# Kernel tuning notes

Measured on AMD Instinct MI355X. Metric: run time of the kernel, lower is better.

The kernel has to match this reference:

```python
import jax, jax.numpy as jnp
import numpy as np

D = 256; DFF = 1024; H = 8; L = 4; P = 4; NK = 18; NQ = 100; BS = 8; DH = D // H
SHAPES = ((100, 100), (50, 50), (25, 25), (13, 13))   # (H_l, W_l) per level
START = (0, 10000, 12500, 13125); LIN = 13294
PARAM_SHAPES = [
    ("across_in_w", (3 * D, D)), ("across_in_b", (3 * D,)), ("across_out_w", (D, D)), ("across_out_b", (D,)),
    ("within_in_w", (3 * D, D)), ("within_in_b", (3 * D,)), ("within_out_w", (D, D)), ("within_out_b", (D,)),
    ("off_w", (H * L * P * 2, D)), ("off_b", (H * L * P * 2,)), ("aw_w", (H * L * P, D)), ("aw_b", (H * L * P,)),
    ("val_w", (D, D)), ("val_b", (D,)), ("msout_w", (D, D)), ("msout_b", (D,)),
    ("lin1_w", (DFF, D)), ("lin1_b", (DFF,)), ("lin2_w", (D, DFF)), ("lin2_b", (D,)),
    ("lin1p_w", (DFF, D)), ("lin1p_b", (DFF,)), ("lin2p_w", (D, DFF)), ("lin2p_b", (D,)),
]
NORMS = ["across_norm", "within_norm", "norm1", "norm2", "norm2p"]
PNAMES = [n for n, _ in PARAM_SHAPES] + [n + s for n in NORMS for s in ("_g", "_b")]


def setup_inputs():
    ks = iter(jax.random.split(jax.random.key(0), 80))
    rn = lambda s, sc=1.0: jax.random.normal(next(ks), s, jnp.float32) * sc
    inp = {}
    inp["tgt_pose"] = rn((NQ, BS, NK, D))
    inp["tgt_pose_query_pos"] = rn((NQ, BS, NK, D))
    inp["tgt_pose_reference_points"] = jax.random.uniform(next(ks), (NQ * NK, BS, L, 2), jnp.float32)
    inp["memory"] = rn((LIN, BS, D))
    for n, s in PARAM_SHAPES:
        inp[n] = rn(s, 0.02)
    for n in NORMS:
        inp[n + "_g"] = 1.0 + rn((D,), 0.02)
        inp[n + "_b"] = rn((D,), 0.02)
    return inp


def _ln(x, g, b):
    mu = x.mean(-1, keepdims=True)
    xc = x - mu
    return xc * jax.lax.rsqrt((xc * xc).mean(-1, keepdims=True) + 1e-5) * g + b


def _mha(q, k, v, in_w, in_b, out_w, out_b, mask=None):
    # q,k,v: [S,B,D] (torch nn.MultiheadAttention layout)
    S, B, _ = q.shape
    def proj(x, i):
        return (x @ in_w[i * D:(i + 1) * D].T + in_b[i * D:(i + 1) * D]).reshape(-1, B, H, DH).transpose(1, 2, 0, 3)
    qh = proj(q, 0) * (DH ** -0.5); kh = proj(k, 1); vh = proj(v, 2)   # [B,H,S,DH]
    sc = jnp.einsum('bhqd,bhkd->bhqk', qh, kh)
    if mask is not None:
        sc = sc + mask
    o = jnp.einsum('bhqk,bhkd->bhqd', jax.nn.softmax(sc, -1), vh)
    return o.transpose(2, 0, 1, 3).reshape(S, B, D) @ out_w.T + out_b


def _msdeform(query, ref, mem, off_w, off_b, aw_w, aw_b, val_w, val_b, out_w, out_b):
    # query [N,Lq,D], ref [N,Lq,L,2] in [0,1] (x,y), mem [N,LIN,D]
    N, Lq, _ = query.shape
    value = (mem @ val_w.T + val_b).reshape(N, LIN, H, DH).transpose(0, 2, 1, 3)   # [N,H,LIN,DH]
    off = (query @ off_w.T + off_b).reshape(N, Lq, H, L, P, 2)
    aw = jax.nn.softmax((query @ aw_w.T + aw_b).reshape(N, Lq, H, L * P), -1).reshape(N, Lq, H, L, P)
    normalizer = jnp.array([[w, h] for (h, w) in SHAPES], jnp.float32)   # (W_l, H_l)
    loc = ref[:, :, None, :, None, :] + off / normalizer[None, None, None, :, None, :]   # [N,Lq,H,L,P,2]
    lvl_outs = []
    for li, (Hl, Wl) in enumerate(SHAPES):
        v_l = value[:, :, START[li]:START[li] + Hl * Wl]   # [N,H,Hl*Wl,DH]
        g = loc[:, :, :, li]                               # [N,Lq,H,P,2]
        # grid_sample(align_corners=False, padding_mode='zeros') on sampling grid 2*loc-1
        x = g[..., 0] * Wl - 0.5; y = g[..., 1] * Hl - 0.5
        x0 = jnp.floor(x); y0 = jnp.floor(y)
        lx = x - x0; ly = y - y0
        x0i = x0.astype(jnp.int32); y0i = y0.astype(jnp.int32)
        def gather(xi, yi):
            valid = ((xi >= 0) & (xi < Wl) & (yi >= 0) & (yi < Hl)).astype(v_l.dtype)
            idx = jnp.clip(yi, 0, Hl - 1) * Wl + jnp.clip(xi, 0, Wl - 1)   # [N,Lq,H,P]
            it = idx.transpose(0, 2, 1, 3).reshape(N, H, Lq * P)
            vt = jnp.take_along_axis(v_l, it[..., None], axis=2).reshape(N, H, Lq, P, DH)
            return vt * valid.transpose(0, 2, 1, 3)[..., None]
        wx = lx.transpose(0, 2, 1, 3)[..., None]; wy = ly.transpose(0, 2, 1, 3)[..., None]
        samp = (gather(x0i, y0i) * (1 - wx) * (1 - wy) + gather(x0i + 1, y0i) * wx * (1 - wy)
                + gather(x0i, y0i + 1) * (1 - wx) * wy + gather(x0i + 1, y0i + 1) * wx * wy)
        lvl_outs.append(samp)   # [N,H,Lq,P,DH]
    samp = jnp.stack(lvl_outs, 0)   # [L,N,H,Lq,P,DH]
    out = jnp.einsum('lnhqpd,nqhlp->nqhd', samp, aw).reshape(N, Lq, D)
    return out @ out_w.T + out_b


def _forward(tgt, pos, ref, mem, p):
    # 1) across-person self-attention along nq
    qf = tgt.reshape(NQ, BS * NK, D)
    t2 = _mha(qf, qf, qf, p['across_in_w'], p['across_in_b'], p['across_out_w'], p['across_out_b']).reshape(NQ, BS, NK, D)
    tgt = _ln(tgt + t2, p['across_norm_g'], p['across_norm_b'])
    # 2) deformable cross-attention; with_pos_embed mutates tgt in place in the original
    tgt = tgt + pos
    q = tgt.transpose(1, 0, 2, 3).reshape(BS, NQ * NK, D)
    t2 = _msdeform(q, ref.transpose(1, 0, 2, 3), mem.transpose(1, 0, 2),
                   p['off_w'], p['off_b'], p['aw_w'], p['aw_b'], p['val_w'], p['val_b'], p['msout_w'], p['msout_b'])
    t2 = t2.reshape(BS, NQ, NK, D).transpose(1, 0, 2, 3)
    tgt = _ln(tgt + t2, p['norm1_g'], p['norm1_b'])
    # 3) FFN
    t2 = jax.nn.relu(tgt @ p['lin1_w'].T + p['lin1_b']) @ p['lin2_w'].T + p['lin2_b']
    tgt = _ln(tgt + t2, p['norm2_g'], p['norm2_b'])
    # 4) within-pose self-attention (second in-place with_pos_embed)
    tgt = tgt + pos
    qw = tgt.reshape(NQ * BS, NK, D).transpose(1, 0, 2)
    mask = jnp.full((NK, NK), 1e-8, tgt.dtype)   # zero adjacency matrix additive mask
    t2 = _mha(qw, qw, qw, p['within_in_w'], p['within_in_b'], p['within_out_w'], p['within_out_b'], mask)
    t2 = t2.transpose(1, 0, 2).reshape(NQ, BS, NK, D)
    tgt = _ln(tgt + t2, p['within_norm_g'], p['within_norm_b'])
    # 5) late FFN
    t2 = jax.nn.relu(tgt @ p['lin1p_w'].T + p['lin1p_b']) @ p['lin2p_w'].T + p['lin2p_b']
    return _ln(tgt + t2, p['norm2p_g'], p['norm2p_b'])


def reference(tgt_pose, tgt_pose_query_pos, tgt_pose_reference_points, memory, across_in_w, across_in_b, across_out_w, across_out_b, within_in_w, within_in_b, within_out_w, within_out_b, off_w, off_b, aw_w, aw_b, val_w, val_b, msout_w, msout_b, lin1_w, lin1_b, lin2_w, lin2_b, lin1p_w, lin1p_b, lin2p_w, lin2p_b, across_norm_g, across_norm_b, within_norm_g, within_norm_b, norm1_g, norm1_b, norm2_g, norm2_b, norm2p_g, norm2p_b):
    _l = dict(locals())
    p = {n: _l[n] for n in PNAMES}
    return _forward(tgt_pose, tgt_pose_query_pos, tgt_pose_reference_points, memory, p)
```

## Files before the change

kernel.cpp:

```cpp
#include <hip/hip_runtime.h>
#include <cstdint>
#include <cstddef>

constexpr int D_   = 256;
constexpr int NK_  = 18;
constexpr int NQ_  = 100;
constexpr int BS_  = 8;
constexpr int T_   = NQ_ * BS_ * NK_;
constexpr int LIN_ = 13294;
constexpr int LQ_  = NQ_ * NK_;

typedef __attribute__((ext_vector_type(8))) short bfv8;
typedef __attribute__((ext_vector_type(4))) float f32x4;

__device__ __forceinline__ ushort f2b(float f) {
  uint32_t u = __builtin_bit_cast(uint32_t, f);
  u += 0x7fffu + ((u >> 16) & 1u);
  return (ushort)(u >> 16);
}
__device__ __forceinline__ float b2f(ushort h) {
  uint32_t u = ((uint32_t)h) << 16;
  return __builtin_bit_cast(float, u);
}
__device__ __forceinline__ uint pk2(float lo, float hi) {
  return (uint)f2b(lo) | ((uint)f2b(hi) << 16);
}
__device__ __forceinline__ void gload16(const ushort* g, ushort* l) {
  __builtin_amdgcn_global_load_lds(
      (const __attribute__((address_space(1))) void*)g,
      (__attribute__((address_space(3))) void*)l, 16, 0, 0);
}

constexpr int WOF0  = 0;
constexpr int WOF1  = 196608;
constexpr int WOF2  = 393216;
constexpr int WOF3  = 458752;
constexpr int WOF4  = 524288;
constexpr int WOF5  = 589824;
constexpr int WOF6  = 622592;
constexpr int WOF7  = 688128;
constexpr int WOF8  = 753664;
constexpr int WOF9  = 1015808;
constexpr int WOF10 = 1277952;
constexpr int WOF11 = 1540096;
constexpr int WTOT  = 1802240;

__global__ __launch_bounds__(256) void conv_weights(
    const float* __restrict__ w0, const float* __restrict__ w1,
    const float* __restrict__ w2, const float* __restrict__ w3,
    const float* __restrict__ w4, const float* __restrict__ w5,
    const float* __restrict__ w6, const float* __restrict__ w7,
    const float* __restrict__ w8, const float* __restrict__ w9,
    const float* __restrict__ w10, const float* __restrict__ w11,
    ushort* __restrict__ out,
    const float* __restrict__ off_b, const float* __restrict__ aw_b,
    float* __restrict__ oab) {
  if (blockIdx.x == 0) {
    int t = threadIdx.x;
    oab[t] = (t < 256) ? off_b[t] : aw_b[t - 256];
    oab[t + 128] = (t + 128 < 256) ? off_b[t + 128] : aw_b[t - 128];
  }
  int i8 = (blockIdx.x * 256 + threadIdx.x) * 8;
  if (i8 >= WTOT) return;
  const float* src; int off;
  if      (i8 < WOF1)  { src = w0;  off = WOF0; }
  else if (i8 < WOF2)  { src = w1;  off = WOF1; }
  else if (i8 < WOF3)  { src = w2;  off = WOF2; }
  else if (i8 < WOF4)  { src = w3;  off = WOF3; }
  else if (i8 < WOF5)  { src = w4;  off = WOF4; }
  else if (i8 < WOF6)  { src = w5;  off = WOF5; }
  else if (i8 < WOF7)  { src = w6;  off = WOF6; }
  else if (i8 < WOF8)  { src = w7;  off = WOF7; }
  else if (i8 < WOF9)  { src = w8;  off = WOF8; }
  else if (i8 < WOF10) { src = w9;  off = WOF9; }
  else if (i8 < WOF11) { src = w10; off = WOF10; }
  else                 { src = w11; off = WOF11; }
  const float4 v0 = *(const float4*)(src + (i8 - off));
  const float4 v1 = *(const float4*)(src + (i8 - off) + 4);
  uint4 o;
  o.x = pk2(v0.x, v0.y); o.y = pk2(v0.z, v0.w);
  o.z = pk2(v1.x, v1.y); o.w = pk2(v1.z, v1.w);
  *(uint4*)(out + i8) = o;
}

__global__ __launch_bounds__(256) void conv_tgt(
    const float* __restrict__ tgt, ushort* __restrict__ tgtb) {
  int idx = blockIdx.x * 256 + threadIdx.x;
  int r = idx >> 5, c = (idx & 31) * 8;
  if (r >= T_) return;
  const float* p = tgt + (size_t)r * 256 + c;
  float4 v0 = *(const float4*)p, v1 = *(const float4*)(p + 4);
  uint4 o;
  o.x = pk2(v0.x, v0.y); o.y = pk2(v0.z, v0.w);
  o.z = pk2(v1.x, v1.y); o.w = pk2(v1.z, v1.w);
  *(uint4*)(tgtb + (size_t)r * 256 + c) = o;
}

__global__ __launch_bounds__(256) void gemm_vproj(
    const float* __restrict__ Amem, const ushort* __restrict__ W,
    const float* __restrict__ bias, ushort* __restrict__ C, int M) {
  __shared__ ushort As[128 * 32];
  __shared__ ushort Bs[128 * 32];
  const int tid = threadIdx.x;
  const int bm = blockIdx.y * 128, bn = blockIdx.x * 128;
  const int wave = tid >> 6, lane = tid & 63;

  const int srow = wave * 16 + (lane >> 2);
  const float* gAf[2]; ushort* lA[2];
  const ushort* gB[2]; ushort* lB[2];
#pragma unroll
  for (int j = 0; j < 2; ++j) {
    int row = j * 64 + srow;
    int gch = (lane & 3) ^ (row & 3);
    int gm = bm + row; if (gm >= M) gm = M - 1;
    gAf[j] = Amem + (size_t)gm * 256 + gch * 8;
    lA[j] = As + (j * 4 + wave) * 512 + lane * 8;
    gB[j] = W + (size_t)(bn + row) * 256 + gch * 8;
    lB[j] = Bs + (j * 4 + wave) * 512;
  }

  const int wm = (wave >> 1) * 64, wn = (wave & 1) * 64;
  const int fr = lane & 15, fk = lane >> 4;
  const int sw = (fk ^ (fr & 3)) << 3;

  float4 ra[2][2];
#pragma unroll
  for (int j = 0; j < 2; ++j) {
    ra[j][0] = *(const float4*)(gAf[j]);
    ra[j][1] = *(const float4*)(gAf[j] + 4);
  }

  f32x4 acc[4][4] = {};
  for (int k0 = 0; k0 < 256; k0 += 32) {
#pragma unroll
    for (int j = 0; j < 2; ++j) gload16(gB[j] + k0, lB[j]);
#pragma unroll
    for (int j = 0; j < 2; ++j) {
      uint4 o;
      o.x = pk2(ra[j][0].x, ra[j][0].y); o.y = pk2(ra[j][0].z, ra[j][0].w);
      o.z = pk2(ra[j][1].x, ra[j][1].y); o.w = pk2(ra[j][1].z, ra[j][1].w);
      *(uint4*)lA[j] = o;
    }
    __syncthreads();
    if (k0 + 32 < 256) {
#pragma unroll
      for (int j = 0; j < 2; ++j) {
        ra[j][0] = *(const float4*)(gAf[j] + k0 + 32);
        ra[j][1] = *(const float4*)(gAf[j] + k0 + 36);
      }
    }
    bfv8 a[4], b[4];
#pragma unroll
    for (int m = 0; m < 4; ++m)
      a[m] = *(const bfv8*)&As[(wm + m * 16 + fr) * 32 + sw];
#pragma unroll
    for (int n = 0; n < 4; ++n)
      b[n] = *(const bfv8*)&Bs[(wn + n * 16 + fr) * 32 + sw];
#pragma unroll
    for (int m = 0; m < 4; ++m)
#pragma unroll
      for (int n = 0; n < 4; ++n)
        acc[m][n] = __builtin_amdgcn_mfma_f32_16x16x32_bf16(a[m], b[n], acc[m][n], 0, 0, 0);
    __syncthreads();
  }

  const int row0 = (lane >> 4) * 4;
  const int col = lane & 15;
#pragma unroll
  for (int m = 0; m < 4; ++m) {
#pragma unroll
    for (int n = 0; n < 4; ++n) {
      int cn = bn + wn + n * 16 + col;
      float bv = bias[cn];
#pragma unroll
      for (int j = 0; j < 4; ++j) {
        int mg = bm + wm + m * 16 + row0 + j;
        if (mg < M) {
          size_t orow = (size_t)(mg & 7) * LIN_ + (mg >> 3);
          C[orow * 256 + cn] = f2b(acc[m][n][j] + bv);
        }
      }
    }
  }
}

template<int AMODE, int OUTMODE, int BM>
__global__ __launch_bounds__(256) void gemm_mfma(
    const ushort* __restrict__ A, const ushort* __restrict__ W,
    const float* __restrict__ bias, void* __restrict__ Cv,
    int M, int N, int K) {
  constexpr int AJ = BM / 64;
  constexpr int MR = BM / 32;
  __shared__ ushort As[BM * 32];
  __shared__ ushort Bs[128 * 32];
  const int tid = threadIdx.x;
  const int bm = blockIdx.y * BM, bn = blockIdx.x * 128;
  const int wave = tid >> 6, lane = tid & 63;

  const int srow = wave * 16 + (lane >> 2);
  const ushort* gA[AJ]; ushort* lA[AJ];
  const ushort* gB[2];  ushort* lB[2];
#pragma unroll
  for (int j = 0; j < AJ; ++j) {
    int row = j * 64 + srow;
    int gch = (lane & 3) ^ (row & 3);
    int gm = bm + row; if (gm >= M) gm = M - 1;
    int asrc;
    if (AMODE == 0) {
      asrc = gm;
    } else {
      int b = gm / LQ_, lq = gm - b * LQ_;
      int qq = lq / NK_, kk = lq - qq * NK_;
      asrc = qq * (BS_ * NK_) + b * NK_ + kk;
    }
    gA[j] = A + (size_t)asrc * K + gch * 8;
    lA[j] = As + (j * 4 + wave) * 512;
  }
#pragma unroll
  for (int j = 0; j < 2; ++j) {
    int row = j * 64 + srow;
    int gch = (lane & 3) ^ (row & 3);
    gB[j] = W + (size_t)(bn + row) * K + gch * 8;
    lB[j] = Bs + (j * 4 + wave) * 512;
  }

  const int wm = (wave >> 1) * (BM / 2), wn = (wave & 1) * 64;
  const int fr = lane & 15, fk = lane >> 4;
  const int sw = (fk ^ (fr & 3)) << 3;

  f32x4 acc[MR][4] = {};
  for (int k0 = 0; k0 < K; k0 += 32) {
#pragma unroll
    for (int j = 0; j < AJ; ++j) gload16(gA[j] + k0, lA[j]);
#pragma unroll
    for (int j = 0; j < 2; ++j) gload16(gB[j] + k0, lB[j]);
    __syncthreads();
    bfv8 a[MR], b[4];
#pragma unroll
    for (int m = 0; m < MR; ++m)
      a[m] = *(const bfv8*)&As[(wm + m * 16 + fr) * 32 + sw];
#pragma unroll
    for (int n = 0; n < 4; ++n)
      b[n] = *(const bfv8*)&Bs[(wn + n * 16 + fr) * 32 + sw];
#pragma unroll
    for (int m = 0; m < MR; ++m)
#pragma unroll
      for (int n = 0; n < 4; ++n)
        acc[m][n] = __builtin_amdgcn_mfma_f32_16x16x32_bf16(a[m], b[n], acc[m][n], 0, 0, 0);
    __syncthreads();
  }

  const int row0 = (lane >> 4) * 4;
  const int col = lane & 15;
#pragma unroll
  for (int m = 0; m < MR; ++m) {
#pragma unroll
    for (int n = 0; n < 4; ++n) {
      int cn = bn + wn + n * 16 + col;
      float bv = bias[cn];
#pragma unroll
      for (int j = 0; j < 4; ++j) {
        int mg = bm + wm + m * 16 + row0 + j;
        if (mg < M) {
          float o = acc[m][n][j] + bv;
          if (OUTMODE == 2) o = fmaxf(o, 0.f);
          if (OUTMODE == 0) ((float*)Cv)[(size_t)mg * N + cn] = o;
          else ((ushort*)Cv)[(size_t)mg * N + cn] = f2b(o);
        }
      }
    }
  }
}

template<int LNMODE>
__global__ __launch_bounds__(256) void gemm_ln(
    const ushort* __restrict__ A, const ushort* __restrict__ W,
    const float* __restrict__ bias, const ushort* __restrict__ Xb,
    const float* __restrict__ POS, const float* __restrict__ G,
    const float* __restrict__ Bb, void* __restrict__ Out, int K) {
  __shared__ float Ep[32][264];
  ushort* As = (ushort*)&Ep[0][0];
  ushort* Bs = As + 32 * 32;

  const int tid = threadIdx.x;
  const int wave = tid >> 6, lane = tid & 63;
  const int bm = blockIdx.x * 32;

  const int arow = wave * 8 + (lane >> 2);
  const int agch = (lane & 3) ^ (arow & 3);
  const ushort* gA = A + (size_t)(bm + arow) * K + agch * 8;
  ushort* lA = As + wave * 256;
  const int srow = wave * 16 + (lane >> 2);
  const ushort* gB[4]; ushort* lB[4];
#pragma unroll
  for (int j = 0; j < 4; ++j) {
    int row = j * 64 + srow;
    int gch = (lane & 3) ^ (row & 3);
    gB[j] = W + (size_t)row * K + gch * 8;
    lB[j] = Bs + (j * 4 + wave) * 512;
  }

  const int wn = wave * 64;
  const int fr = lane & 15, fk = lane >> 4;
  const int sw = (fk ^ (fr & 3)) << 3;

  f32x4 acc[2][4] = {};
  for (int k0 = 0; k0 < K; k0 += 32) {
    if (lane < 32) gload16(gA + k0, lA);
#pragma unroll
    for (int j = 0; j < 4; ++j) gload16(gB[j] + k0, lB[j]);
    __syncthreads();
    bfv8 a[2], b[4];
#pragma unroll
    for (int m = 0; m < 2; ++m)
      a[m] = *(const bfv8*)&As[(m * 16 + fr) * 32 + sw];
#pragma unroll
    for (int n = 0; n < 4; ++n)
      b[n] = *(const bfv8*)&Bs[(wn + n * 16 + fr) * 32 + sw];
#pragma unroll
    for (int m = 0; m < 2; ++m)
#pragma unroll
      for (int n = 0; n < 4; ++n)
        acc[m][n] = __builtin_amdgcn_mfma_f32_16x16x32_bf16(a[m], b[n], acc[m][n], 0, 0, 0);
    __syncthreads();
  }

  const int row0 = (lane >> 4) * 4;
  const int col = lane & 15;
  float bv[4];
#pragma unroll
  for (int n = 0; n < 4; ++n) bv[n] = bias[wn + n * 16 + col];

  const float4 g4 = *(const float4*)(G + lane * 4);
  const float4 bb4 = *(const float4*)(Bb + lane * 4);

#pragma unroll
  for (int m = 0; m < 2; ++m)
#pragma unroll
    for (int n = 0; n < 4; ++n)
#pragma unroll
      for (int j = 0; j < 4; ++j)
        Ep[m * 16 + row0 + j][wn + n * 16 + col] = acc[m][n][j] + bv[n];
  __syncthreads();

  for (int rr = 0; rr < 8; ++rr) {
    int lrow = wave * 8 + rr;
    size_t off = (size_t)(bm + lrow) * 256 + lane * 4;
    float4 ev = *(const float4*)&Ep[lrow][lane * 4];
    ushort4 x4 = *(const ushort4*)(Xb + off);
    float4 v = make_float4(b2f(x4.x) + ev.x, b2f(x4.y) + ev.y,
                           b2f(x4.z) + ev.z, b2f(x4.w) + ev.w);
    float s = v.x + v.y + v.z + v.w;
#pragma unroll
    for (int o = 32; o; o >>= 1) s += __shfl_xor(s, o);
    float mu = s * (1.0f / 256.0f);
    float4 c = make_float4(v.x - mu, v.y - mu, v.z - mu, v.w - mu);
    float q = c.x * c.x + c.y * c.y + c.z * c.z + c.w * c.w;
#pragma unroll
    for (int o = 32; o; o >>= 1) q += __shfl_xor(q, o);
    float rs = rsqrtf(q * (1.0f / 256.0f) + 1e-5f);
    float4 o4;
    o4.x = c.x * rs * g4.x + bb4.x;
    o4.y = c.y * rs * g4.y + bb4.y;
    o4.z = c.z * rs * g4.z + bb4.z;
    o4.w = c.w * rs * g4.w + bb4.w;
    if (LNMODE == 0) {
      float4 pv = *(const float4*)(POS + off);
      o4.x += pv.x; o4.y += pv.y; o4.z += pv.z; o4.w += pv.w;
    }
    if (LNMODE == 2) {
      *(float4*)((float*)Out + off) = o4;
    } else {
      ushort4 ob;
      ob.x = f2b(o4.x); ob.y = f2b(o4.y); ob.z = f2b(o4.z); ob.w = f2b(o4.w);
      *(ushort4*)((ushort*)Out + off) = ob;
    }
  }
}

__global__ __launch_bounds__(256) void attn_across_mfma(
    const ushort* __restrict__ QKV, ushort* __restrict__ O) {
  __shared__ ushort Qs[112][40];
  __shared__ ushort Ks[112][40];
  __shared__ ushort Vt[32][136];
  __shared__ ushort Ps[112][136];
  const int b = blockIdx.x >> 3, h = blockIdx.x & 7;
  const int tid = threadIdx.x;

  for (int idx = tid; idx < 112 * 16; idx += 256) {
    int r = idx >> 4, du = (idx & 15) * 2;
    uint q = 0, k = 0;
    if (r < 100) {
      size_t base = ((size_t)r * 144 + b) * 768 + h * 32 + du;
      q = *(const uint*)(QKV + base);
      k = *(const uint*)(QKV + base + 256);
    }
    *(uint*)&Qs[r][du] = q;
    *(uint*)&Ks[r][du] = k;
  }
  for (int idx = tid; idx < 128 * 32; idx += 256) {
    int s = idx >> 5, d = idx & 31;
    ushort v = 0;
    if (s < 100) v = QKV[((size_t)s * 144 + b) * 768 + 512 + h * 32 + d];
    Vt[d][s] = v;
  }
  for (int idx = tid; idx < 112 * 8; idx += 256) {
    int r = idx >> 3, c = 112 + (idx & 7) * 2;
    *(uint*)&Ps[r][c] = 0;
  }
  __syncthreads();

  const int wave = tid >> 6, lane = tid & 63;
  const int fr = lane & 15, fk = lane >> 4;
  const float scale = 0.17677669529663687f;

#pragma unroll
  for (int mi = 0; mi < 2; ++mi) {
    const int mt = wave + mi * 4;
    if (mt < 7) {
      bfv8 aq = *(const bfv8*)&Qs[mt * 16 + fr][fk * 8];
      f32x4 sacc[7];
#pragma unroll
      for (int nt = 0; nt < 7; ++nt) {
        bfv8 bk = *(const bfv8*)&Ks[nt * 16 + fr][fk * 8];
        f32x4 z = {0.f, 0.f, 0.f, 0.f};
        sacc[nt] = __builtin_amdgcn_mfma_f32_16x16x32_bf16(aq, bk, z, 0, 0, 0);
      }
      const bool maskc = (lane & 15) >= 4;
#pragma unroll
      for (int j = 0; j < 4; ++j) {
        float v[7];
        float mx = -1e30f;
#pragma unroll
        for (int nt = 0; nt < 7; ++nt) {
          float s = sacc[nt][j] * scale;
          if (nt == 6 && maskc) s = -1e30f;
          v[nt] = s;
          mx = fmaxf(mx, s);
        }
        mx = fmaxf(mx, __shfl_xor(mx, 1));
        mx = fmaxf(mx, __shfl_xor(mx, 2));
        mx = fmaxf(mx, __shfl_xor(mx, 4));
        mx = fmaxf(mx, __shfl_xor(mx, 8));
        float sum = 0.f;
#pragma unroll
        for (int nt = 0; nt < 7; ++nt) {
          v[nt] = __expf(v[nt] - mx);
          sum += v[nt];
        }
        sum += __shfl_xor(sum, 1);
        sum += __shfl_xor(sum, 2);
        sum += __shfl_xor(sum, 4);
        sum += __shfl_xor(sum, 8);
        float inv = 1.f / sum;
        int row = mt * 16 + (lane >> 4) * 4 + j;
#pragma unroll
        for (int nt = 0; nt < 7; ++nt)
          Ps[row][nt * 16 + (lane & 15)] = f2b(v[nt] * inv);
      }
    }
  }
  __syncthreads();

  f32x4 oacc[2][2] = {};
#pragma unroll
  for (int mi = 0; mi < 2; ++mi) {
    const int mt = wave + mi * 4;
    if (mt < 7) {
#pragma unroll
      for (int ks = 0; ks < 4; ++ks) {
        bfv8 ap = *(const bfv8*)&Ps[mt * 16 + fr][ks * 32 + fk * 8];
#pragma unroll
        for (int n = 0; n < 2; ++n) {
          bfv8 bv = *(const bfv8*)&Vt[n * 16 + fr][ks * 32 + fk * 8];
          oacc[mi][n] = __builtin_amdgcn_mfma_f32_16x16x32_bf16(ap, bv, oacc[mi][n], 0, 0, 0);
        }
      }
#pragma unroll
      for (int n = 0; n < 2; ++n) {
#pragma unroll
        for (int j = 0; j < 4; ++j) {
          int q = mt * 16 + (lane >> 4) * 4 + j;
          if (q < 100) {
            O[((size_t)q * 144 + b) * 256 + h * 32 + n * 16 + (lane & 15)] =
                f2b(oacc[mi][n][j]);
          }
        }
      }
    }
  }
}

__global__ __launch_bounds__(256) void attn_within(
    const ushort* __restrict__ QKV, ushort* __restrict__ O) {
  constexpr int ST = 258;
  __shared__ ushort Qs[18 * ST];
  __shared__ ushort Ks[18 * ST];
  __shared__ ushort Vs[18 * ST];
  const int bidx = blockIdx.x;
  const int qq = bidx >> 3, bb = bidx & 7;
  const int tid = threadIdx.x;
  for (int idx = tid; idx < 18 * 128; idx += 256) {
    int r = idx >> 7, j2 = (idx & 127) * 2;
    size_t base = ((size_t)qq * 144 + bb * 18 + r) * 768 + j2;
    *(uint*)&Qs[r * ST + j2] = *(const uint*)(QKV + base);
    *(uint*)&Ks[r * ST + j2] = *(const uint*)(QKV + base + 256);
    *(uint*)&Vs[r * ST + j2] = *(const uint*)(QKV + base + 512);
  }
  __syncthreads();
  const int wave = tid >> 6, lane = tid & 63;
  const int h = wave * 2 + (lane >> 5);
  const int li = lane & 31;
  const int hd = h * 32;
  const float scale = 0.17677669529663687f;
  const bool kv = li < 18;
  for (int s = 0; s < 18; ++s) {
    float sc = 0.f;
    if (kv) {
      const ushort* qrow = &Qs[s * ST + hd];
      const ushort* krow = &Ks[li * ST + hd];
#pragma unroll 8
      for (int d = 0; d < 32; ++d) sc += b2f(qrow[d]) * b2f(krow[d]);
    }
    sc = kv ? sc * scale : -1e30f;
    float mx = sc;
    mx = fmaxf(mx, __shfl_xor(mx, 16));
    mx = fmaxf(mx, __shfl_xor(mx, 8));
    mx = fmaxf(mx, __shfl_xor(mx, 4));
    mx = fmaxf(mx, __shfl_xor(mx, 2));
    mx = fmaxf(mx, __shfl_xor(mx, 1));
    float e = kv ? __expf(sc - mx) : 0.f;
    float sum = e;
    sum += __shfl_xor(sum, 16);
    sum += __shfl_xor(sum, 8);
    sum += __shfl_xor(sum, 4);
    sum += __shfl_xor(sum, 2);
    sum += __shfl_xor(sum, 1);
    float p = e / sum;
    float o = 0.f;
    const int half = lane & 32;
#pragma unroll
    for (int k = 0; k < 18; ++k) {
      float pk = __shfl(p, half + k);
      o += pk * b2f(Vs[k * ST + hd + li]);
    }
    O[((size_t)qq * 144 + bb * 18 + s) * 256 + hd + li] = f2b(o);
  }
}

__global__ __launch_bounds__(256) void deform_sample(
    const float* __restrict__ OFFAW, const ushort* __restrict__ V,
    const float* __restrict__ REF, ushort* __restrict__ OUT) {
  __shared__ uint2 sDesc[32 * 65];
  const int tid = threadIdx.x;
  const int m0 = blockIdx.x * 4;

  const int WH[4] = {100, 50, 25, 13};
  const int STl[4] = {0, 10000, 12500, 13125};

#pragma unroll
  for (int dd = 0; dd < 2; ++dd) {
    const int desc = tid + dd * 256;
    const int g = desc >> 7, rem = desc & 127;
    const int h = rem >> 4, lp = rem & 15, li = lp >> 2, p = lp & 3;
    const int m = m0 + g;
    const int b = m / LQ_, lq = m - b * LQ_;

    float awv = OFFAW[(size_t)m * 384 + 256 + h * 16 + lp];
    float mx = awv;
    mx = fmaxf(mx, __shfl_xor(mx, 8, 16));
    mx = fmaxf(mx, __shfl_xor(mx, 4, 16));
    mx = fmaxf(mx, __shfl_xor(mx, 2, 16));
    mx = fmaxf(mx, __shfl_xor(mx, 1, 16));
    float e = __expf(awv - mx);
    float sm = e;
    sm += __shfl_xor(sm, 8, 16);
    sm += __shfl_xor(sm, 4, 16);
    sm += __shfl_xor(sm, 2, 16);
    sm += __shfl_xor(sm, 1, 16);
    const float aw = e / sm;

    const float* offp = OFFAW + (size_t)m * 384 + h * 32 + li * 8 + p * 2;
    const float ox = offp[0], oy = offp[1];
    const float rx = REF[(((size_t)lq * 8 + b) * 4 + li) * 2 + 0];
    const float ry = REF[(((size_t)lq * 8 + b) * 4 + li) * 2 + 1];
    const int Wl = WH[li], st = STl[li];
    const float fW = (float)Wl;
    const float x = fmaf(rx, fW, ox) - 0.5f;
    const float y = fmaf(ry, fW, oy) - 0.5f;
    const float x0f = floorf(x), y0f = floorf(y);
    const float lx = x - x0f, ly = y - y0f;
    const int x0 = (int)x0f, y0 = (int)y0f;
    const int base = (g * 8 + h) * 65 + lp * 4;
#pragma unroll
    for (int c = 0; c < 4; ++c) {
      const int cx = c & 1, cy = c >> 1;
      const int xi = x0 + cx, yi = y0 + cy;
      const bool va = (xi >= 0) && (xi < Wl) && (yi >= 0) && (yi < Wl);
      const int xc = min(max(xi, 0), Wl - 1);
      const int yc = min(max(yi, 0), Wl - 1);
      const float wx = cx ? lx : (1.f - lx);
      const float wy = cy ? ly : (1.f - ly);
      const float wgt = va ? aw * wx * wy : 0.f;
      uint2 dv;
      dv.x = (uint)(st + yc * Wl + xc);
      dv.y = __builtin_bit_cast(uint, wgt);
      sDesc[base + c] = dv;
    }
  }
  __syncthreads();

  const int g = tid >> 6;
  const int h = (tid >> 3) & 7;
  const int d4 = (tid & 7) * 4;
  const int m = m0 + g;
  const int b = m / LQ_, lq = m - b * LQ_;
  const int qq = lq / NK_, kk = lq - qq * NK_;
  const ushort* Vg = V + ((size_t)b * LIN_) * 256 + h * 32 + d4;
  const int dbase = (g * 8 + h) * 65;
  float a0 = 0.f, a1 = 0.f, a2 = 0.f, a3 = 0.f;
#pragma unroll
  for (int lp = 0; lp < 16; ++lp) {
#pragma unroll
    for (int c = 0; c < 4; ++c) {
      const uint2 dv = sDesc[dbase + lp * 4 + c];
      const float w = __builtin_bit_cast(float, dv.y);
      const ushort4 v = *(const ushort4*)(Vg + (size_t)dv.x * 256);
      a0 = fmaf(w, b2f(v.x), a0);
      a1 = fmaf(w, b2f(v.y), a1);
      a2 = fmaf(w, b2f(v.z), a2);
      a3 = fmaf(w, b2f(v.w), a3);
    }
  }
  const size_t tok = (size_t)qq * 144 + b * 18 + kk;
  ushort4 o;
  o.x = f2b(a0); o.y = f2b(a1); o.z = f2b(a2); o.w = f2b(a3);
  *(ushort4*)(OUT + tok * 256 + h * 32 + d4) = o;
}

extern "C" void kernel_launch(void* const* d_in, const int* in_sizes, int n_in,
                              void* d_out, int out_size, void* d_ws, size_t ws_size,
                              hipStream_t stream) {
  const float* tgt  = (const float*)d_in[0];
  const float* pos  = (const float*)d_in[1];
  const float* ref  = (const float*)d_in[2];
  const float* mem  = (const float*)d_in[3];
  const float* across_in_w  = (const float*)d_in[4];
  const float* across_in_b  = (const float*)d_in[5];
  const float* across_out_w = (const float*)d_in[6];
  const float* across_out_b = (const float*)d_in[7];
  const float* within_in_w  = (const float*)d_in[8];
  const float* within_in_b  = (const float*)d_in[9];
  const float* within_out_w = (const float*)d_in[10];
  const float* within_out_b = (const float*)d_in[11];
  const float* off_w  = (const float*)d_in[12];
  const float* off_b  = (const float*)d_in[13];
  const float* aw_w   = (const float*)d_in[14];
  const float* aw_b   = (const float*)d_in[15];
  const float* val_w  = (const float*)d_in[16];
  const float* val_b  = (const float*)d_in[17];
  const float* msout_w = (const float*)d_in[18];
  const float* msout_b = (const float*)d_in[19];
  const float* lin1_w  = (const float*)d_in[20];
  const float* lin1_b  = (const float*)d_in[21];
  const float* lin2_w  = (const float*)d_in[22];
  const float* lin2_b  = (const float*)d_in[23];
  const float* lin1p_w = (const float*)d_in[24];
  const float* lin1p_b = (const float*)d_in[25];
  const float* lin2p_w = (const float*)d_in[26];
  const float* lin2p_b = (const float*)d_in[27];
  const float* across_norm_g = (const float*)d_in[28];
  const float* across_norm_b = (const float*)d_in[29];
  const float* within_norm_g = (const float*)d_in[30];
  const float* within_norm_b = (const float*)d_in[31];
  const float* norm1_g = (const float*)d_in[32];
  const float* norm1_b = (const float*)d_in[33];
  const float* norm2_g = (const float*)d_in[34];
  const float* norm2_b = (const float*)d_in[35];
  const float* norm2p_g = (const float*)d_in[36];
  const float* norm2p_b = (const float*)d_in[37];

  char* w = (char*)d_ws;
  ushort* Wb    = (ushort*)w;  w += 3604480;
  ushort* QKVb  = (ushort*)w;  w += (size_t)(BS_ * LIN_) * 256 * 2;
  ushort* AOb   = (ushort*)w;  w += (size_t)T_ * 256 * 2;
  ushort* CTb   = (ushort*)w;  w += (size_t)T_ * 256 * 2;
  ushort* Vb    = (ushort*)w;  w += (size_t)(BS_ * LIN_) * 256 * 2;
  float*  R2    = (float*)w;   w += (size_t)T_ * 384 * 4;
  float*  OAB   = (float*)w;   w += 384 * 4;
  ushort* tgtb  = (ushort*)R2;
  float*  OFFAW = R2;
  ushort* Uff   = Vb;
  ushort* SMPb  = AOb;

  ushort* W_across_in  = Wb + WOF0;
  ushort* W_within_in  = Wb + WOF1;
  ushort* W_across_out = Wb + WOF2;
  ushort* W_within_out = Wb + WOF3;
  ushort* W_offaw      = Wb + WOF4;
  ushort* W_val        = Wb + WOF6;
  ushort* W_msout      = Wb + WOF7;
  ushort* W_lin1       = Wb + WOF8;
  ushort* W_lin2       = Wb + WOF9;
  ushort* W_lin1p      = Wb + WOF10;
  ushort* W_lin2p      = Wb + WOF11;

  dim3 blk(256);
  const int MT = T_;
  const int MV = BS_ * LIN_;
  const int MVt = (MV + 127) / 128;
  const int MT64 = MT / 64;
  const int MT32 = MT / 32;

  conv_weights<<<dim3((WTOT / 8 + 255) / 256), blk, 0, stream>>>(
      across_in_w, within_in_w, across_out_w, within_out_w, off_w, aw_w,
      val_w, msout_w, lin1_w, lin2_w, lin1p_w, lin2p_w, Wb, off_b, aw_b, OAB);
  conv_tgt<<<dim3(MT * 32 / 256), blk, 0, stream>>>(tgt, tgtb);
  gemm_vproj<<<dim3(2, MVt), blk, 0, stream>>>(
      mem, W_val, val_b, Vb, MV);
  gemm_mfma<0, 1, 64><<<dim3(6, MT64), blk, 0, stream>>>(
      tgtb, W_across_in, across_in_b, QKVb, MT, 768, 256);
  attn_across_mfma<<<dim3(144 * 8), blk, 0, stream>>>(QKVb, AOb);
  gemm_ln<0><<<dim3(MT32), blk, 0, stream>>>(
      AOb, W_across_out, across_out_b, tgtb, pos,
      across_norm_g, across_norm_b, CTb, 256);
  gemm_mfma<2, 0, 64><<<dim3(3, MT64), blk, 0, stream>>>(
      CTb, W_offaw, OAB, OFFAW, MT, 384, 256);
  deform_sample<<<dim3(T_ / 4), blk, 0, stream>>>(OFFAW, Vb, ref, SMPb);
  gemm_ln<1><<<dim3(MT32), blk, 0, stream>>>(
      SMPb, W_msout, msout_b, CTb, nullptr,
      norm1_g, norm1_b, CTb, 256);
  gemm_mfma<0, 2, 64><<<dim3(8, MT64), blk, 0, stream>>>(
      CTb, W_lin1, lin1_b, Uff, MT, 1024, 256);
  gemm_ln<0><<<dim3(MT32), blk, 0, stream>>>(
      Uff, W_lin2, lin2_b, CTb, pos,
      norm2_g, norm2_b, CTb, 1024);
  gemm_mfma<0, 1, 64><<<dim3(6, MT64), blk, 0, stream>>>(
      CTb, W_within_in, within_in_b, QKVb, MT, 768, 256);
  attn_within<<<dim3(NQ_ * BS_), blk, 0, stream>>>(QKVb, AOb);
  gemm_ln<1><<<dim3(MT32), blk, 0, stream>>>(
      AOb, W_within_out, within_out_b, CTb, nullptr,
      within_norm_g, within_norm_b, CTb, 256);
  gemm_mfma<0, 2, 64><<<dim3(8, MT64), blk, 0, stream>>>(
      CTb, W_lin1p, lin1p_b, Uff, MT, 1024, 256);
  gemm_ln<2><<<dim3(MT32), blk, 0, stream>>>(
      Uff, W_lin2p, lin2p_b, CTb, nullptr,
      norm2p_g, norm2p_b, (float*)d_out, 1024);
}
```

Before: 371.1 us.

## Preload full weight tile into LDS and double-buffer A in value-projection GEMM

The value-projection GEMM now loads the whole 128x256 bf16 weight slab into shared memory once, using an XOR swizzle, instead of streaming 32-wide K slices. The fp32 activation tile is double-buffered in LDS with two-stage register prefetch, so each K step needs one barrier instead of two. This cuts per-iteration global weight loads and synchronisation, at the cost of much larger LDS use (about 80KB), which may reduce occupancy. It also relies on a manual lgkmcnt wait plus raw s_barrier being enough for the async gload16 of B to finish.

```diff
diff --git a/kernel.cpp b/kernel.cpp
--- a/kernel.cpp
+++ b/kernel.cpp
@@ -99,69 +99,85 @@
 __global__ __launch_bounds__(256) void gemm_vproj(
     const float* __restrict__ Amem, const ushort* __restrict__ W,
     const float* __restrict__ bias, ushort* __restrict__ C, int M) {
-  __shared__ ushort As[128 * 32];
-  __shared__ ushort Bs[128 * 32];
+  __shared__ ushort As[2][128 * 32];
+  __shared__ ushort Bs[128 * 256];
   const int tid = threadIdx.x;
   const int bm = blockIdx.y * 128, bn = blockIdx.x * 128;
   const int wave = tid >> 6, lane = tid & 63;
 
   const int srow = wave * 16 + (lane >> 2);
-  const float* gAf[2]; ushort* lA[2];
-  const ushort* gB[2]; ushort* lB[2];
+  const float* gAf[2]; int lAoff[2];
 #pragma unroll
   for (int j = 0; j < 2; ++j) {
     int row = j * 64 + srow;
     int gch = (lane & 3) ^ (row & 3);
     int gm = bm + row; if (gm >= M) gm = M - 1;
     gAf[j] = Amem + (size_t)gm * 256 + gch * 8;
-    lA[j] = As + (j * 4 + wave) * 512 + lane * 8;
-    gB[j] = W + (size_t)(bn + row) * 256 + gch * 8;
-    lB[j] = Bs + (j * 4 + wave) * 512;
-  }
+    lAoff[j] = (j * 4 + wave) * 512 + lane * 8;
+  }
+
+  float4 ra[2][2][2];
+#pragma unroll
+  for (int j = 0; j < 2; ++j) {
+    ra[0][j][0] = *(const float4*)(gAf[j]);
+    ra[0][j][1] = *(const float4*)(gAf[j] + 4);
+    ra[1][j][0] = *(const float4*)(gAf[j] + 32);
+    ra[1][j][1] = *(const float4*)(gAf[j] + 36);
+  }
+#pragma unroll
+  for (int j2 = 0; j2 < 16; ++j2) {
+    int u = (j2 * 4 + wave) * 64 + lane;
+    int row = u >> 5, c = u & 31;
+    int gcol = (((c >> 2) ^ (row & 7)) << 5) + (((c & 3) ^ (row & 3)) << 3);
+    gload16(W + (size_t)(bn + row) * 256 + gcol,
+            &Bs[(size_t)(j2 * 4 + wave) * 512]);
+  }
+  __syncthreads();
 
   const int wm = (wave >> 1) * 64, wn = (wave & 1) * 64;
   const int fr = lane & 15, fk = lane >> 4;
   const int sw = (fk ^ (fr & 3)) << 3;
 
-  float4 ra[2][2];
-#pragma unroll
-  for (int j = 0; j < 2; ++j) {
-    ra[j][0] = *(const float4*)(gAf[j]);
-    ra[j][1] = *(const float4*)(gAf[j] + 4);
-  }
-
   f32x4 acc[4][4] = {};
-  for (int k0 = 0; k0 < 256; k0 += 32) {
-#pragma unroll
-    for (int j = 0; j < 2; ++j) gload16(gB[j] + k0, lB[j]);
+#pragma unroll
+  for (int k = 0; k < 8; ++k) {
+    const int buf = k & 1;
+    ushort* asb = &As[buf][0];
 #pragma unroll
     for (int j = 0; j < 2; ++j) {
       uint4 o;
-      o.x = pk2(ra[j][0].x, ra[j][0].y); o.y = pk2(ra[j][0].z, ra[j][0].w);
-      o.z = pk2(ra[j][1].x, ra[j][1].y); o.w = pk2(ra[j][1].z, ra[j][1].w);
-      *(uint4*)lA[j] = o;
-    }
-    __syncthreads();
-    if (k0 + 32 < 256) {
+      o.x = pk2(ra[buf][j][0].x, ra[buf][j][0].y);
+      o.y = pk2(ra[buf][j][0].z, ra[buf][j][0].w);
+      o.z = pk2(ra[buf][j][1].x, ra[buf][j][1].y);
+      o.w = pk2(ra[buf][j][1].z, ra[buf][j][1].w);
+      *(uint4*)(asb + lAoff[j]) = o;
+    }
+    if (k < 6) {
 #pragma unroll
       for (int j = 0; j < 2; ++j) {
-        ra[j][0] = *(const float4*)(gAf[j] + k0 + 32);
-        ra[j][1] = *(const float4*)(gAf[j] + k0 + 36);
+        ra[buf][j][0] = *(const float4*)(gAf[j] + (k + 2) * 32);
+        ra[buf][j][1] = *(const float4*)(gAf[j] + (k + 2) * 32 + 4);
       }
     }
+    asm volatile("s_waitcnt lgkmcnt(0)" ::: "memory");
+    __builtin_amdgcn_s_barrier();
+    __builtin_amdgcn_sched_barrier(0);
+
     bfv8 a[4], b[4];
 #pragma unroll
     for (int m = 0; m < 4; ++m)
-      a[m] = *(const bfv8*)&As[(wm + m * 16 + fr) * 32 + sw];
-#pragma unroll
-    for (int n = 0; n < 4; ++n)
-      b[n] = *(const bfv8*)&Bs[(wn + n * 16 + fr) * 32 + sw];
+      a[m] = *(const bfv8*)&asb[(wm + m * 16 + fr) * 32 + sw];
+#pragma unroll
+    for (int n = 0; n < 4; ++n) {
+      int r = wn + n * 16 + fr;
+      int c = ((k ^ (r & 7)) << 2) | (fk ^ (r & 3));
+      b[n] = *(const bfv8*)&Bs[r * 256 + c * 8];
+    }
 #pragma unroll
     for (int m = 0; m < 4; ++m)
 #pragma unroll
       for (int n = 0; n < 4; ++n)
         acc[m][n] = __builtin_amdgcn_mfma_f32_16x16x32_bf16(a[m], b[n], acc[m][n], 0, 0, 0);
-    __syncthreads();
   }
 
   const int row0 = (lane >> 4) * 4;
```

New measurement: 379.4 us. 2.2% more time.

## Fuse value projection and across-attention in-projection into one interleaved launch

Applied to the files above, without the earlier changes.

Merges the independent memory value-projection GEMM and the across-attention QKV in-projection GEMM into a single kernel. Block IDs are interleaved so the two kinds of tiles run side by side on the GPU. This removes one launch and the tail or serialization gap between two independent GEMMs. The cost is a larger, branchy kernel whose register and LDS use is sized for the heavier branch, which could lower occupancy for the in-projection tiles.

```diff
diff --git a/kernel.cpp b/kernel.cpp
--- a/kernel.cpp
+++ b/kernel.cpp
@@ -96,88 +96,159 @@
   *(uint4*)(tgtb + (size_t)r * 256 + c) = o;
 }
 
-__global__ __launch_bounds__(256) void gemm_vproj(
-    const float* __restrict__ Amem, const ushort* __restrict__ W,
-    const float* __restrict__ bias, ushort* __restrict__ C, int M) {
-  __shared__ ushort As[128 * 32];
-  __shared__ ushort Bs[128 * 32];
+constexpr int NVB = 2 * 831;
+constexpr int NIB = 6 * 225;
+
+__global__ __launch_bounds__(256) void vproj_inproj(
+    const float* __restrict__ Amem, const ushort* __restrict__ Wv,
+    const float* __restrict__ vbias, ushort* __restrict__ Cv, int MV,
+    const ushort* __restrict__ At, const ushort* __restrict__ Wi,
+    const float* __restrict__ ibias, ushort* __restrict__ Ci) {
+  __shared__ ushort SH[8192];
+  const int bid = blockIdx.x;
   const int tid = threadIdx.x;
-  const int bm = blockIdx.y * 128, bn = blockIdx.x * 128;
   const int wave = tid >> 6, lane = tid & 63;
 
-  const int srow = wave * 16 + (lane >> 2);
-  const float* gAf[2]; ushort* lA[2];
-  const ushort* gB[2]; ushort* lB[2];
-#pragma unroll
-  for (int j = 0; j < 2; ++j) {
-    int row = j * 64 + srow;
-    int gch = (lane & 3) ^ (row & 3);
-    int gm = bm + row; if (gm >= M) gm = M - 1;
-    gAf[j] = Amem + (size_t)gm * 256 + gch * 8;
-    lA[j] = As + (j * 4 + wave) * 512 + lane * 8;
-    gB[j] = W + (size_t)(bn + row) * 256 + gch * 8;
-    lB[j] = Bs + (j * 4 + wave) * 512;
-  }
-
-  const int wm = (wave >> 1) * 64, wn = (wave & 1) * 64;
+  bool isv; int sub;
+  if (bid < 2 * NIB) { isv = !(bid & 1); sub = bid >> 1; }
+  else               { isv = true; sub = NIB + (bid - 2 * NIB); }
+
   const int fr = lane & 15, fk = lane >> 4;
   const int sw = (fk ^ (fr & 3)) << 3;
-
-  float4 ra[2][2];
-#pragma unroll
-  for (int j = 0; j < 2; ++j) {
-    ra[j][0] = *(const float4*)(gAf[j]);
-    ra[j][1] = *(const float4*)(gAf[j] + 4);
-  }
-
-  f32x4 acc[4][4] = {};
-  for (int k0 = 0; k0 < 256; k0 += 32) {
-#pragma unroll
-    for (int j = 0; j < 2; ++j) gload16(gB[j] + k0, lB[j]);
-#pragma unroll
-    for (int j = 0; j < 2; ++j) {
-      uint4 o;
-      o.x = pk2(ra[j][0].x, ra[j][0].y); o.y = pk2(ra[j][0].z, ra[j][0].w);
-      o.z = pk2(ra[j][1].x, ra[j][1].y); o.w = pk2(ra[j][1].z, ra[j][1].w);
-      *(uint4*)lA[j] = o;
-    }
-    __syncthreads();
-    if (k0 + 32 < 256) {
-#pragma unroll
-      for (int j = 0; j < 2; ++j) {
-        ra[j][0] = *(const float4*)(gAf[j] + k0 + 32);
-        ra[j][1] = *(const float4*)(gAf[j] + k0 + 36);
-      }
-    }
-    bfv8 a[4], b[4];
-#pragma unroll
-    for (int m = 0; m < 4; ++m)
-      a[m] = *(const bfv8*)&As[(wm + m * 16 + fr) * 32 + sw];
-#pragma unroll
-    for (int n = 0; n < 4; ++n)
-      b[n] = *(const bfv8*)&Bs[(wn + n * 16 + fr) * 32 + sw];
-#pragma unroll
-    for (int m = 0; m < 4; ++m)
-#pragma unroll
-      for (int n = 0; n < 4; ++n)
-        acc[m][n] = __builtin_amdgcn_mfma_f32_16x16x32_bf16(a[m], b[n], acc[m][n], 0, 0, 0);
-    __syncthreads();
-  }
-
+  const int srow = wave * 16 + (lane >> 2);
   const int row0 = (lane >> 4) * 4;
   const int col = lane & 15;
-#pragma unroll
-  for (int m = 0; m < 4; ++m) {
-#pragma unroll
-    for (int n = 0; n < 4; ++n) {
-      int cn = bn + wn + n * 16 + col;
-      float bv = bias[cn];
-#pragma unroll
-      for (int j = 0; j < 4; ++j) {
-        int mg = bm + wm + m * 16 + row0 + j;
-        if (mg < M) {
-          size_t orow = (size_t)(mg & 7) * LIN_ + (mg >> 3);
-          C[orow * 256 + cn] = f2b(acc[m][n][j] + bv);
+
+  if (isv) {
+    ushort* As = SH;
+    ushort* Bs = SH + 4096;
+    const int bm = (sub >> 1) * 128, bn = (sub & 1) * 128;
+
+    const float* gAf[2]; ushort* lA[2];
+    const ushort* gB[2]; ushort* lB[2];
+#pragma unroll
+    for (int j = 0; j < 2; ++j) {
+      int row = j * 64 + srow;
+      int gch = (lane & 3) ^ (row & 3);
+      int gm = bm + row; if (gm >= MV) gm = MV - 1;
+      gAf[j] = Amem + (size_t)gm * 256 + gch * 8;
+      lA[j] = As + (j * 4 + wave) * 512 + lane * 8;
+      gB[j] = Wv + (size_t)(bn + row) * 256 + gch * 8;
+      lB[j] = Bs + (j * 4 + wave) * 512;
+    }
+
+    const int wm = (wave >> 1) * 64, wn = (wave & 1) * 64;
+
+    float4 ra[2][2];
+#pragma unroll
+    for (int j = 0; j < 2; ++j) {
+      ra[j][0] = *(const float4*)(gAf[j]);
+      ra[j][1] = *(const float4*)(gAf[j] + 4);
+    }
+
+    f32x4 acc[4][4] = {};
+    for (int k0 = 0; k0 < 256; k0 += 32) {
+#pragma unroll
+      for (int j = 0; j < 2; ++j) gload16(gB[j] + k0, lB[j]);
+#pragma unroll
+      for (int j = 0; j < 2; ++j) {
+        uint4 o;
+        o.x = pk2(ra[j][0].x, ra[j][0].y); o.y = pk2(ra[j][0].z, ra[j][0].w);
+        o.z = pk2(ra[j][1].x, ra[j][1].y); o.w = pk2(ra[j][1].z, ra[j][1].w);
+        *(uint4*)lA[j] = o;
+      }
+      __syncthreads();
+      if (k0 + 32 < 256) {
+#pragma unroll
+        for (int j = 0; j < 2; ++j) {
+          ra[j][0] = *(const float4*)(gAf[j] + k0 + 32);
+          ra[j][1] = *(const float4*)(gAf[j] + k0 + 36);
+        }
+      }
+      bfv8 a[4], b[4];
+#pragma unroll
+      for (int m = 0; m < 4; ++m)
+        a[m] = *(const bfv8*)&As[(wm + m * 16 + fr) * 32 + sw];
+#pragma unroll
+      for (int n = 0; n < 4; ++n)
+        b[n] = *(const bfv8*)&Bs[(wn + n * 16 + fr) * 32 + sw];
+#pragma unroll
+      for (int m = 0; m < 4; ++m)
+#pragma unroll
+        for (int n = 0; n < 4; ++n)
+          acc[m][n] = __builtin_amdgcn_mfma_f32_16x16x32_bf16(a[m], b[n], acc[m][n], 0, 0, 0);
+      __syncthreads();
+    }
+
+#pragma unroll
+    for (int m = 0; m < 4; ++m) {
+#pragma unroll
+      for (int n = 0; n < 4; ++n) {
+        int cn = bn + wn + n * 16 + col;
+        float bv = vbias[cn];
+#pragma unroll
+        for (int j = 0; j < 4; ++j) {
+          int mg = bm + wm + m * 16 + row0 + j;
+          if (mg < MV) {
+            size_t orow = (size_t)(mg & 7) * LIN_ + (mg >> 3);
+            Cv[orow * 256 + cn] = f2b(acc[m][n][j] + bv);
+          }
+        }
+      }
+    }
+  } else {
+    ushort* As = SH;
+    ushort* Bs = SH + 2048;
+    const int bm = (sub / 6) * 64, bn = (sub % 6) * 128;
+
+    const ushort* gA; ushort* lA;
+    const ushort* gB[2]; ushort* lB[2];
+    {
+      int gch = (lane & 3) ^ (srow & 3);
+      gA = At + (size_t)(bm + srow) * 256 + gch * 8;
+      lA = As + wave * 512;
+    }
+#pragma unroll
+    for (int j = 0; j < 2; ++j) {
+      int row = j * 64 + srow;
+      int gch = (lane & 3) ^ (row & 3);
+      gB[j] = Wi + (size_t)(bn + row) * 256 + gch * 8;
+      lB[j] = Bs + (j * 4 + wave) * 512;
+    }
+
+    const int wm = (wave >> 1) * 32, wn = (wave & 1) * 64;
+
+    f32x4 acc[2][4] = {};
+    for (int k0 = 0; k0 < 256; k0 += 32) {
+      gload16(gA + k0, lA);
+#pragma unroll
+      for (int j = 0; j < 2; ++j) gload16(gB[j] + k0, lB[j]);
+      __syncthreads();
+      bfv8 a[2], b[4];
+#pragma unroll
+      for (int m = 0; m < 2; ++m)
+        a[m] = *(const bfv8*)&As[(wm + m * 16 + fr) * 32 + sw];
+#pragma unroll
+      for (int n = 0; n < 4; ++n)
+        b[n] = *(const bfv8*)&Bs[(wn + n * 16 + fr) * 32 + sw];
+#pragma unroll
+      for (int m = 0; m < 2; ++m)
+#pragma unroll
+        for (int n = 0; n < 4; ++n)
+          acc[m][n] = __builtin_amdgcn_mfma_f32_16x16x32_bf16(a[m], b[n], acc[m][n], 0, 0, 0);
+      __syncthreads();
+    }
+
+#pragma unroll
+    for (int m = 0; m < 2; ++m) {
+#pragma unroll
+      for (int n = 0; n < 4; ++n) {
+        int cn = bn + wn + n * 16 + col;
+        float bv = ibias[cn];
+#pragma unroll
+        for (int j = 0; j < 4; ++j) {
+          int mg = bm + wm + m * 16 + row0 + j;
+          Ci[(size_t)mg * 768 + cn] = f2b(acc[m][n][j] + bv);
         }
       }
     }
@@ -708,7 +779,6 @@
   dim3 blk(256);
   const int MT = T_;
   const int MV = BS_ * LIN_;
-  const int MVt = (MV + 127) / 128;
   const int MT64 = MT / 64;
   const int MT32 = MT / 32;
 
@@ -716,10 +786,9 @@
       across_in_w, within_in_w, across_out_w, within_out_w, off_w, aw_w,
       val_w, msout_w, lin1_w, lin2_w, lin1p_w, lin2p_w, Wb, off_b, aw_b, OAB);
   conv_tgt<<<dim3(MT * 32 / 256), blk, 0, stream>>>(tgt, tgtb);
-  gemm_vproj<<<dim3(2, MVt), blk, 0, stream>>>(
-      mem, W_val, val_b, Vb, MV);
-  gemm_mfma<0, 1, 64><<<dim3(6, MT64), blk, 0, stream>>>(
-      tgtb, W_across_in, across_in_b, QKVb, MT, 768, 256);
+  vproj_inproj<<<dim3(NVB + NIB), blk, 0, stream>>>(
+      mem, W_val, val_b, Vb, MV,
+      tgtb, W_across_in, across_in_b, QKVb);
   attn_across_mfma<<<dim3(144 * 8), blk, 0, stream>>>(QKVb, AOb);
   gemm_ln<0><<<dim3(MT32), blk, 0, stream>>>(
       AOb, W_across_out, across_out_b, tgtb, pos,
```

Measured after the change: 395.6 us. +6.6%, slower.
